# Optimization experiments

Hardware: AMD Instinct MI355X
Metric: run time of the kernel (lower is better)

The kernel has to match this reference:

```python
import jax, jax.numpy as jnp
import numpy as np

N_ENTITY = 64368
N_REL = 40
DIM = 128
NUM_BASES = 8
N_EDGES = 1_200_000
BATCH = 64
MAX_SEED = 32


def setup_inputs() -> dict:
    key = jax.random.key(0)
    ks = jax.random.split(key, 12)
    basis = jax.random.normal(ks[0], (NUM_BASES, N_ENTITY, DIM), jnp.float32) * 0.02
    att = jax.random.normal(ks[1], (N_REL, NUM_BASES), jnp.float32) * 0.1
    root = jax.random.normal(ks[2], (N_ENTITY, DIM), jnp.float32) * 0.02
    rgcn_bias = jnp.zeros((DIM,), jnp.float32)
    xav = 1.414 / np.sqrt(DIM)  # xavier_uniform gain=1.414 scale
    attn_a = jax.random.uniform(ks[3], (DIM, DIM), jnp.float32, -xav, xav)
    attn_b = jax.random.uniform(ks[4], (DIM, 1), jnp.float32, -xav, xav)
    output_bias = jnp.zeros((N_ENTITY,), jnp.float32)
    edge_index = jax.random.randint(ks[5], (2, N_EDGES), 0, N_ENTITY, jnp.int32)
    edge_type = jax.random.randint(ks[6], (N_EDGES,), 0, N_REL, jnp.int32)
    lengths = jax.random.randint(ks[7], (BATCH,), 1, MAX_SEED + 1, jnp.int32)
    seed_mask = jnp.arange(MAX_SEED)[None, :] < lengths[:, None]  # ragged seed sets
    seed_idx = jax.random.randint(ks[8], (BATCH, MAX_SEED), 0, N_ENTITY, jnp.int32)
    labels = jax.random.randint(ks[9], (BATCH,), 0, N_ENTITY, jnp.int32)
    return dict(basis=basis, att=att, root=root, rgcn_bias=rgcn_bias,
                attn_a=attn_a, attn_b=attn_b, output_bias=output_bias,
                edge_index=edge_index, edge_type=edge_type,
                seed_idx=seed_idx, seed_mask=seed_mask, labels=labels)


def reference(basis, att, root, rgcn_bias, attn_a, attn_b, output_bias,
              edge_index, edge_type, seed_idx, seed_mask, labels):
    # ---- RGCNConv with x=None (old PyG): msg_e = (att[rel_e] @ basis)[src_e] ----
    src, dst = edge_index[0], edge_index[1]
    coeff = att[edge_type]                      # [E, B]
    # loop over small fixed num_bases to avoid materializing [B, E, D]
    msg = coeff[:, 0:1] * basis[0][src]         # [E, D]
    for b in range(1, basis.shape[0]):
        msg = msg + coeff[:, b:b + 1] * basis[b][src]
    agg = jax.ops.segment_sum(msg, dst, num_segments=root.shape[0])  # scatter-add
    nodes = agg + root + rgcn_bias              # [N, D] node features

    # ---- per-seed-set gather + self-attention pooling ----
    h = nodes[seed_idx]                         # [Bt, L, D]
    e = jnp.squeeze(jnp.tanh(h @ attn_a) @ attn_b, -1)  # [Bt, L]
    e = jnp.where(seed_mask, e, -jnp.inf)
    attn = jax.nn.softmax(e, axis=-1)
    u = jnp.einsum('bl,bld->bd', attn, h)       # [Bt, D] user reps

    # ---- scores = F.linear(u, nodes, output.bias); CE loss ----
    scores = u @ nodes.T + output_bias          # [Bt, N]
    logp = jax.nn.log_softmax(scores, axis=-1)
    loss = -jnp.mean(jnp.take_along_axis(logp, labels[:, None].astype(jnp.int32), axis=1))
    return scores, loss
```

## Files before the change

kernel.cpp:

```cpp
#include <hip/hip_runtime.h>
#include <hip/hip_bf16.h>

#define N_ENT 64368
#define DIM 128
#define NB 8
#define NREL 40
#define BATCH 64
#define MAXSEED 32

__device__ __forceinline__ unsigned pack_bf2(float x, float y) {
    union { float f; unsigned u; } a, b;
    a.f = x; b.f = y;
    unsigned ra = a.u + 0x7FFFu + ((a.u >> 16) & 1u);
    unsigned rb = b.u + 0x7FFFu + ((b.u >> 16) & 1u);
    return (ra >> 16) | (rb & 0xFFFF0000u);
}

__global__ void mask_norm_kernel(const unsigned char* __restrict__ raw,
                                 int* __restrict__ outMask) {
    __shared__ int s_ni, s_nf;
    int t = threadIdx.x;
    if (t == 0) { s_ni = 0; s_nf = 0; }
    __syncthreads();
    const unsigned int* u32 = (const unsigned int*)raw;
    int not_int = 0, not_flt = 0;
    for (int i = t; i < 512; i += blockDim.x) {
        unsigned int g = u32[i];
        if (g != 0u && g != 1u) not_int = 1;
        if (g != 0u && g != 0x3F800000u) not_flt = 1;
    }
    if (not_int) atomicOr(&s_ni, 1);
    if (not_flt) atomicOr(&s_nf, 1);
    __syncthreads();
    int mode = (!s_ni) ? 0 : ((!s_nf) ? 1 : 2);
    for (int i = t; i < BATCH * MAXSEED; i += blockDim.x) {
        int v;
        if (mode == 0)      v = ((const int*)raw)[i] != 0;
        else if (mode == 1) v = (((const float*)raw)[i] != 0.0f);
        else                v = raw[i] != 0;
        outMask[i] = v;
    }
}

__global__ __launch_bounds__(256) void hist_kernel(
    const int* __restrict__ eidx, int E,
    int* __restrict__ cntS, int* __restrict__ cntD)
{
    int i = blockIdx.x * blockDim.x + threadIdx.x;
    int n = gridDim.x * blockDim.x;
    for (int e = i; e < E; e += n) {
        atomicAdd(&cntS[eidx[e]], 1);
        atomicAdd(&cntD[eidx[e + E]], 1);
    }
}

__global__ __launch_bounds__(1024) void scan2_kernel(
    const int* __restrict__ cntS, int* __restrict__ rpS, int* __restrict__ ofS,
    const int* __restrict__ cntD, int* __restrict__ rpD, int* __restrict__ ofD)
{
    const int* cnt = blockIdx.x ? cntD : cntS;
    int* row_ptr   = blockIdx.x ? rpD : rpS;
    int* ofs       = blockIdx.x ? ofD : ofS;
    __shared__ int s[1024];
    const int t = threadIdx.x;
    const int CH = 63;
    const int base = t * CH;
    int sum = 0;
    for (int j = 0; j < CH; ++j) { int p = base + j; if (p < N_ENT) sum += cnt[p]; }
    s[t] = sum;
    for (int off = 1; off < 1024; off <<= 1) {
        __syncthreads();
        int x = (t >= off) ? s[t - off] : 0;
        __syncthreads();
        s[t] += x;
    }
    __syncthreads();
    int run = s[t] - sum;
    for (int j = 0; j < CH; ++j) {
        int p = base + j;
        if (p < N_ENT) { row_ptr[p] = run; ofs[p] = run; run += cnt[p]; }
    }
    if (t == 1023) row_ptr[N_ENT] = s[1023];
}

__global__ __launch_bounds__(256) void scat2_kernel(
    const int* __restrict__ eidx, const int* __restrict__ etype, int E,
    int* __restrict__ ofsS, int* __restrict__ ofsD, int useDstRank,
    unsigned* __restrict__ srcSorted)
{
    int i = blockIdx.x * blockDim.x + threadIdx.x;
    int n = gridDim.x * blockDim.x;
    for (int e = i; e < E; e += n) {
        int s = eidx[e];
        int d = eidx[e + E];
        int p = atomicAdd(&ofsS[s], 1);
        unsigned hi = useDstRank ? (unsigned)atomicAdd(&ofsD[d], 1) : (unsigned)d;
        srcSorted[p] = (hi << 6) | (unsigned)etype[e];
    }
}

__global__ __launch_bounds__(256) void msg_kernel(
    const float* __restrict__ basis, const float* __restrict__ att,
    const int* __restrict__ row_ptrS, const unsigned* __restrict__ srcSorted,
    unsigned* __restrict__ msg)
{
    __shared__ float att_s[NREL * NB];
    const int t = threadIdx.x;
    for (int i = t; i < NREL * NB; i += 256) att_s[i] = att[i];
    __syncthreads();
    const int lane = t & 63;
    const int s = blockIdx.x * 4 + (t >> 6);
    const int r0 = row_ptrS[s], r1 = row_ptrS[s + 1];
    if (r0 == r1) return;
    float2 B[NB];
#pragma unroll
    for (int b = 0; b < NB; ++b)
        B[b] = ((const float2*)(basis + ((size_t)b * N_ENT + s) * DIM))[lane];
    for (int i = r0; i < r1; ++i) {
        unsigned pk = srcSorted[i];
        const float* __restrict__ c = att_s + (pk & 63u) * NB;
        size_t dp = (size_t)(pk >> 6);
        float mx = 0.f, my = 0.f;
#pragma unroll
        for (int b = 0; b < NB; ++b) { mx += c[b] * B[b].x; my += c[b] * B[b].y; }
        __builtin_nontemporal_store(pack_bf2(mx, my), msg + dp * 64 + lane);
    }
}

__global__ __launch_bounds__(256) void reduce_kernel(
    const unsigned* __restrict__ msg, const int* __restrict__ row_ptrD,
    const float* __restrict__ root, const float* __restrict__ rbias,
    float* __restrict__ nodes)
{
    const int t = threadIdx.x;
    const int lane = t & 63;
    const int d = blockIdx.x * 4 + (t >> 6);
    const int r0 = row_ptrD[d], r1 = row_ptrD[d + 1];
    float2 acc = ((const float2*)(root + (size_t)d * DIM))[lane];
    acc.x += rbias[lane * 2];
    acc.y += rbias[lane * 2 + 1];
    for (int i = r0; i < r1; ++i) {
        unsigned u = __builtin_nontemporal_load(msg + (size_t)i * 64 + lane);
        acc.x += __uint_as_float(u << 16);
        acc.y += __uint_as_float(u & 0xFFFF0000u);
    }
    ((float2*)(nodes + (size_t)d * DIM))[lane] = acc;
}

__global__ __launch_bounds__(256) void edge_atomic_kernel(
    const float* __restrict__ basis, const float* __restrict__ att,
    const int* __restrict__ row_ptrS, const unsigned* __restrict__ srcSorted,
    float* __restrict__ nodes)
{
    __shared__ float att_s[NREL * NB];
    const int t = threadIdx.x;
    for (int i = t; i < NREL * NB; i += 256) att_s[i] = att[i];
    __syncthreads();
    const int lane = t & 63;
    const int s = blockIdx.x * 4 + (t >> 6);
    const int r0 = row_ptrS[s], r1 = row_ptrS[s + 1];
    if (r0 == r1) return;
    float2 B[NB];
#pragma unroll
    for (int b = 0; b < NB; ++b)
        B[b] = ((const float2*)(basis + ((size_t)b * N_ENT + s) * DIM))[lane];
    for (int i = r0; i < r1; ++i) {
        unsigned pk = srcSorted[i];
        const float* __restrict__ c = att_s + (pk & 63u) * NB;
        int d = (int)(pk >> 6);
        float mx = 0.f, my = 0.f;
#pragma unroll
        for (int b = 0; b < NB; ++b) { mx += c[b] * B[b].x; my += c[b] * B[b].y; }
        float* dp = nodes + (size_t)d * DIM + lane * 2;
        unsafeAtomicAdd(dp, mx);
        unsafeAtomicAdd(dp + 1, my);
    }
}

__global__ __launch_bounds__(256) void finalize_nodes(
    float* __restrict__ nodes, const float* __restrict__ root,
    const float* __restrict__ bias, int total)
{
    int i = blockIdx.x * blockDim.x + threadIdx.x;
    if (i < total) nodes[i] = nodes[i] + root[i] + bias[i & (DIM - 1)];
}

__global__ __launch_bounds__(128) void attn_kernel(
    const float* __restrict__ nodes, const float* __restrict__ A,
    const float* __restrict__ bvec, const int* __restrict__ seed_idx,
    const int* __restrict__ maskN, float* __restrict__ u)
{
    __shared__ float A_s[DIM * DIM];
    __shared__ float h_s[MAXSEED * DIM];
    __shared__ float ev[MAXSEED];
    __shared__ float aw[MAXSEED];
    __shared__ float red[2];
    const int b = blockIdx.x;
    const int t = threadIdx.x;

    for (int i = t; i < DIM * DIM; i += 128) A_s[i] = A[i];
    for (int l = 0; l < MAXSEED; ++l) {
        int idx = seed_idx[b * MAXSEED + l];
        h_s[l * DIM + t] = nodes[(size_t)idx * DIM + t];
    }
    __syncthreads();

    const float bv = bvec[t];
    for (int l = 0; l < MAXSEED; ++l) {
        float s = 0.f;
#pragma unroll 8
        for (int d1 = 0; d1 < DIM; ++d1) s += h_s[l * DIM + d1] * A_s[d1 * DIM + t];
        float val = tanhf(s) * bv;
#pragma unroll
        for (int off = 32; off > 0; off >>= 1) val += __shfl_down(val, off, 64);
        if ((t & 63) == 0) red[t >> 6] = val;
        __syncthreads();
        if (t == 0) ev[l] = red[0] + red[1];
        __syncthreads();
    }

    if (t == 0) {
        float mx = -1e30f;
        for (int l = 0; l < MAXSEED; ++l)
            if (maskN[b * MAXSEED + l]) mx = fmaxf(mx, ev[l]);
        float den = 0.f;
        for (int l = 0; l < MAXSEED; ++l) {
            float w = maskN[b * MAXSEED + l] ? expf(ev[l] - mx) : 0.f;
            aw[l] = w;
            den += w;
        }
        float inv = 1.f / den;
        for (int l = 0; l < MAXSEED; ++l) aw[l] *= inv;
    }
    __syncthreads();

    float s = 0.f;
    for (int l = 0; l < MAXSEED; ++l) s += aw[l] * h_s[l * DIM + t];
    u[b * DIM + t] = s;
}

__global__ __launch_bounds__(256) void scores_kernel(
    const float* __restrict__ nodes, const float* __restrict__ u,
    const float* __restrict__ obias, float* __restrict__ out)
{
    __shared__ float u_s[BATCH * DIM];
    const int t = threadIdx.x;
    const int n0 = blockIdx.x * 64;
    for (int i = t; i < BATCH * DIM; i += 256) u_s[i] = u[i];
    __syncthreads();
    const int nl = t & 63, bg = t >> 6;
    const int n = n0 + nl;
    const int nc = n < N_ENT ? n : N_ENT - 1;
    const float4* __restrict__ nrow = (const float4*)(nodes + (size_t)nc * DIM);
    float acc[16];
#pragma unroll
    for (int bi = 0; bi < 16; ++bi) acc[bi] = 0.f;
    for (int dc = 0; dc < DIM / 4; ++dc) {
        const float4 nr = nrow[dc];
#pragma unroll
        for (int bi = 0; bi < 16; ++bi) {
            const float4 uu = *(const float4*)(u_s + (bg * 16 + bi) * DIM + dc * 4);
            acc[bi] += nr.x * uu.x + nr.y * uu.y + nr.z * uu.z + nr.w * uu.w;
        }
    }
    if (n < N_ENT) {
        const float ob = obias[n];
#pragma unroll
        for (int bi = 0; bi < 16; ++bi)
            out[(size_t)(bg * 16 + bi) * N_ENT + n] = acc[bi] + ob;
    }
}

#define LSE_CH 8
__global__ __launch_bounds__(256) void lse1_kernel(
    const float* __restrict__ scores, float2* __restrict__ pls)
{
    const int b = blockIdx.x >> 3, c = blockIdx.x & 7;
    const int t = threadIdx.x;
    const int CH = (N_ENT + LSE_CH - 1) / LSE_CH;
    const int i0 = c * CH, i1 = min(N_ENT, i0 + CH);
    const float* __restrict__ row = scores + (size_t)b * N_ENT;
    __shared__ float red[4], red2[4];
    float mx = -1e30f;
    for (int i = i0 + t; i < i1; i += 256) mx = fmaxf(mx, row[i]);
#pragma unroll
    for (int off = 32; off > 0; off >>= 1) mx = fmaxf(mx, __shfl_down(mx, off, 64));
    if ((t & 63) == 0) red[t >> 6] = mx;
    __syncthreads();
    const float m4 = fmaxf(fmaxf(red[0], red[1]), fmaxf(red[2], red[3]));
    float ss = 0.f;
    for (int i = i0 + t; i < i1; i += 256) ss += expf(row[i] - m4);
#pragma unroll
    for (int off = 32; off > 0; off >>= 1) ss += __shfl_down(ss, off, 64);
    if ((t & 63) == 0) red2[t >> 6] = ss;
    __syncthreads();
    if (t == 0) pls[blockIdx.x] = make_float2(m4, red2[0] + red2[1] + red2[2] + red2[3]);
}

__global__ void lse2_kernel(const float2* __restrict__ pls, float* __restrict__ lse)
{
    const int b = threadIdx.x;
    if (b < BATCH) {
        float M = -1e30f;
        for (int c = 0; c < LSE_CH; ++c) M = fmaxf(M, pls[b * LSE_CH + c].x);
        float S = 0.f;
        for (int c = 0; c < LSE_CH; ++c) {
            float2 p = pls[b * LSE_CH + c];
            S += p.y * expf(p.x - M);
        }
        lse[b] = M + logf(S);
    }
}

__global__ void loss_kernel(const float* __restrict__ scores,
                            const float* __restrict__ lse,
                            const int* __restrict__ labels,
                            float* __restrict__ out_loss)
{
    const int t = threadIdx.x;
    float v = 0.f;
    if (t < BATCH) {
        int lab = labels[t];
        v = lse[t] - scores[(size_t)t * N_ENT + lab];
    }
#pragma unroll
    for (int off = 32; off > 0; off >>= 1) v += __shfl_down(v, off, 64);
    if (t == 0) out_loss[0] = v * (1.0f / BATCH);
}

extern "C" void kernel_launch(void* const* d_in, const int* in_sizes, int n_in,
                              void* d_out, int out_size, void* d_ws, size_t ws_size,
                              hipStream_t stream) {
    const float* basis = (const float*)d_in[0];
    const float* att   = (const float*)d_in[1];
    const float* root  = (const float*)d_in[2];
    const float* rbias = (const float*)d_in[3];
    const float* attnA = (const float*)d_in[4];
    const float* attnB = (const float*)d_in[5];
    const float* obias = (const float*)d_in[6];
    const int* eindex  = (const int*)d_in[7];
    const int* etype   = (const int*)d_in[8];
    const int* sidx    = (const int*)d_in[9];
    const unsigned char* smask = (const unsigned char*)d_in[10];
    const int* labels  = (const int*)d_in[11];
    const int E = in_sizes[8];
    float* out = (float*)d_out;

    auto alignup = [](size_t x) { return (x + 511) & ~(size_t)511; };
    char* p = (char*)d_ws;
    float* nodes = (float*)p;      p += alignup((size_t)N_ENT * DIM * 4);
    float* u     = (float*)p;      p += alignup((size_t)BATCH * DIM * 4);
    float* lse   = (float*)p;      p += alignup(BATCH * 4);
    float2* pls  = (float2*)p;     p += alignup(BATCH * LSE_CH * 8);
    int* maskN   = (int*)p;        p += alignup(BATCH * MAXSEED * 4);
    int* cntS    = (int*)p;
    int* cntD    = cntS + N_ENT;   p += alignup((size_t)2 * N_ENT * 4);
    int* row_ptrS= (int*)p;        p += alignup((size_t)(N_ENT + 1) * 4);
    int* ofsS    = (int*)p;        p += alignup((size_t)N_ENT * 4);
    int* row_ptrD= (int*)p;        p += alignup((size_t)(N_ENT + 1) * 4);
    int* ofsD    = (int*)p;        p += alignup((size_t)N_ENT * 4);
    unsigned* srcSorted = (unsigned*)p; p += alignup((size_t)E * 4);
    unsigned* msg = (unsigned*)p;  p += alignup((size_t)E * 64 * 4);
    const bool planA = ((size_t)(p - (char*)d_ws) <= ws_size);

    const int eb = (E + 255) / 256;
    const int egrid = eb > 2048 ? 2048 : eb;

    mask_norm_kernel<<<1, 256, 0, stream>>>(smask, maskN);
    hipMemsetAsync(cntS, 0, (size_t)2 * N_ENT * 4, stream);
    hist_kernel<<<egrid, 256, 0, stream>>>(eindex, E, cntS, cntD);
    scan2_kernel<<<2, 1024, 0, stream>>>(cntS, row_ptrS, ofsS, cntD, row_ptrD, ofsD);

    if (planA) {
        scat2_kernel<<<egrid, 256, 0, stream>>>(eindex, etype, E, ofsS, ofsD, 1, srcSorted);
        msg_kernel<<<N_ENT / 4, 256, 0, stream>>>(basis, att, row_ptrS, srcSorted, msg);
        reduce_kernel<<<N_ENT / 4, 256, 0, stream>>>(msg, row_ptrD, root, rbias, nodes);
    } else {
        hipMemsetAsync(nodes, 0, (size_t)N_ENT * DIM * 4, stream);
        scat2_kernel<<<egrid, 256, 0, stream>>>(eindex, etype, E, ofsS, ofsD, 0, srcSorted);
        edge_atomic_kernel<<<N_ENT / 4, 256, 0, stream>>>(basis, att, row_ptrS, srcSorted, nodes);
        finalize_nodes<<<((N_ENT * DIM) + 255) / 256, 256, 0, stream>>>(nodes, root, rbias, N_ENT * DIM);
    }

    attn_kernel<<<BATCH, 128, 0, stream>>>(nodes, attnA, attnB, sidx, maskN, u);
    scores_kernel<<<(N_ENT + 63) / 64, 256, 0, stream>>>(nodes, u, obias, out);
    lse1_kernel<<<BATCH * LSE_CH, 256, 0, stream>>>(out, pls);
    lse2_kernel<<<1, 64, 0, stream>>>(pls, lse);
    loss_kernel<<<1, 64, 0, stream>>>(out, lse, labels, out + (size_t)BATCH * N_ENT);
}
```

Baseline: 1.114 ms.

## Pad offset counters, vectorize edge loads, move dst-rank atomics into msg kernel

Offset counters are padded to 64 bytes apart so that atomics on different nodes no longer contend on the same cache line. The histogram and scatter kernels now handle four edges per thread with int4 loads. The destination-rank atomic moves out of the scatter pass into the message kernel, where one lane per edge claims the slot and the result is shuffled to the wavefront. This removes one atomic per edge from scatter, but puts atomic latency on the msg kernel's critical path, and the padded counters take 16x more memory.

```diff
diff --git a/kernel.cpp b/kernel.cpp
--- a/kernel.cpp
+++ b/kernel.cpp
@@ -7,6 +7,7 @@
 #define NREL 40
 #define BATCH 64
 #define MAXSEED 32
+#define OPAD 16
 
 __device__ __forceinline__ unsigned pack_bf2(float x, float y) {
     union { float f; unsigned u; } a, b;
@@ -46,11 +47,20 @@
     const int* __restrict__ eidx, int E,
     int* __restrict__ cntS, int* __restrict__ cntD)
 {
-    int i = blockIdx.x * blockDim.x + threadIdx.x;
-    int n = gridDim.x * blockDim.x;
-    for (int e = i; e < E; e += n) {
-        atomicAdd(&cntS[eidx[e]], 1);
-        atomicAdd(&cntD[eidx[e + E]], 1);
+    const int t = blockIdx.x * blockDim.x + threadIdx.x;
+    const int e0 = t * 4;
+    if (((E & 3) == 0) && e0 + 3 < E) {
+        int4 s4 = *(const int4*)(eidx + e0);
+        int4 d4 = *(const int4*)(eidx + E + e0);
+        atomicAdd(&cntS[s4.x], 1); atomicAdd(&cntS[s4.y], 1);
+        atomicAdd(&cntS[s4.z], 1); atomicAdd(&cntS[s4.w], 1);
+        atomicAdd(&cntD[d4.x], 1); atomicAdd(&cntD[d4.y], 1);
+        atomicAdd(&cntD[d4.z], 1); atomicAdd(&cntD[d4.w], 1);
+    } else {
+        for (int e = e0; e < E && e < e0 + 4; ++e) {
+            atomicAdd(&cntS[eidx[e]], 1);
+            atomicAdd(&cntD[eidx[e + E]], 1);
+        }
     }
 }
 
@@ -78,31 +88,41 @@
     int run = s[t] - sum;
     for (int j = 0; j < CH; ++j) {
         int p = base + j;
-        if (p < N_ENT) { row_ptr[p] = run; ofs[p] = run; run += cnt[p]; }
+        if (p < N_ENT) { row_ptr[p] = run; ofs[(size_t)p * OPAD] = run; run += cnt[p]; }
     }
     if (t == 1023) row_ptr[N_ENT] = s[1023];
 }
 
-__global__ __launch_bounds__(256) void scat2_kernel(
+__global__ __launch_bounds__(256) void scatS_kernel(
     const int* __restrict__ eidx, const int* __restrict__ etype, int E,
-    int* __restrict__ ofsS, int* __restrict__ ofsD, int useDstRank,
-    unsigned* __restrict__ srcSorted)
-{
-    int i = blockIdx.x * blockDim.x + threadIdx.x;
-    int n = gridDim.x * blockDim.x;
-    for (int e = i; e < E; e += n) {
-        int s = eidx[e];
-        int d = eidx[e + E];
-        int p = atomicAdd(&ofsS[s], 1);
-        unsigned hi = useDstRank ? (unsigned)atomicAdd(&ofsD[d], 1) : (unsigned)d;
-        srcSorted[p] = (hi << 6) | (unsigned)etype[e];
+    int* __restrict__ ofsS, unsigned* __restrict__ srcSorted)
+{
+    const int t = blockIdx.x * blockDim.x + threadIdx.x;
+    const int e0 = t * 4;
+    if (((E & 3) == 0) && e0 + 3 < E) {
+        int4 s4 = *(const int4*)(eidx + e0);
+        int4 d4 = *(const int4*)(eidx + E + e0);
+        int4 r4 = *(const int4*)(etype + e0);
+        int p0 = atomicAdd(&ofsS[(size_t)s4.x * OPAD], 1);
+        int p1 = atomicAdd(&ofsS[(size_t)s4.y * OPAD], 1);
+        int p2 = atomicAdd(&ofsS[(size_t)s4.z * OPAD], 1);
+        int p3 = atomicAdd(&ofsS[(size_t)s4.w * OPAD], 1);
+        srcSorted[p0] = ((unsigned)d4.x << 6) | (unsigned)r4.x;
+        srcSorted[p1] = ((unsigned)d4.y << 6) | (unsigned)r4.y;
+        srcSorted[p2] = ((unsigned)d4.z << 6) | (unsigned)r4.z;
+        srcSorted[p3] = ((unsigned)d4.w << 6) | (unsigned)r4.w;
+    } else {
+        for (int e = e0; e < E && e < e0 + 4; ++e) {
+            int p = atomicAdd(&ofsS[(size_t)eidx[e] * OPAD], 1);
+            srcSorted[p] = ((unsigned)eidx[e + E] << 6) | (unsigned)etype[e];
+        }
     }
 }
 
 __global__ __launch_bounds__(256) void msg_kernel(
     const float* __restrict__ basis, const float* __restrict__ att,
     const int* __restrict__ row_ptrS, const unsigned* __restrict__ srcSorted,
-    unsigned* __restrict__ msg)
+    int* __restrict__ ofsD, unsigned* __restrict__ msg)
 {
     __shared__ float att_s[NREL * NB];
     const int t = threadIdx.x;
@@ -116,14 +136,20 @@
 #pragma unroll
     for (int b = 0; b < NB; ++b)
         B[b] = ((const float2*)(basis + ((size_t)b * N_ENT + s) * DIM))[lane];
-    for (int i = r0; i < r1; ++i) {
-        unsigned pk = srcSorted[i];
-        const float* __restrict__ c = att_s + (pk & 63u) * NB;
-        size_t dp = (size_t)(pk >> 6);
-        float mx = 0.f, my = 0.f;
-#pragma unroll
-        for (int b = 0; b < NB; ++b) { mx += c[b] * B[b].x; my += c[b] * B[b].y; }
-        __builtin_nontemporal_store(pack_bf2(mx, my), msg + dp * 64 + lane);
+    for (int i = r0; i < r1; i += 4) {
+        const int m = min(4, r1 - i);
+        unsigned pk_l = (lane < m) ? srcSorted[i + lane] : 0u;
+        int q_l = 0;
+        if (lane < m) q_l = atomicAdd(&ofsD[(size_t)(pk_l >> 6) * OPAD], 1);
+        for (int j = 0; j < m; ++j) {
+            unsigned pk = (unsigned)__shfl((int)pk_l, j, 64);
+            int q = __shfl(q_l, j, 64);
+            const float* __restrict__ c = att_s + (pk & 63u) * NB;
+            float mx = 0.f, my = 0.f;
+#pragma unroll
+            for (int b = 0; b < NB; ++b) { mx += c[b] * B[b].x; my += c[b] * B[b].y; }
+            __builtin_nontemporal_store(pack_bf2(mx, my), msg + (size_t)q * 64 + lane);
+        }
     }
 }
 
@@ -356,28 +382,26 @@
     int* cntS    = (int*)p;
     int* cntD    = cntS + N_ENT;   p += alignup((size_t)2 * N_ENT * 4);
     int* row_ptrS= (int*)p;        p += alignup((size_t)(N_ENT + 1) * 4);
-    int* ofsS    = (int*)p;        p += alignup((size_t)N_ENT * 4);
     int* row_ptrD= (int*)p;        p += alignup((size_t)(N_ENT + 1) * 4);
-    int* ofsD    = (int*)p;        p += alignup((size_t)N_ENT * 4);
+    int* ofsS    = (int*)p;        p += alignup((size_t)N_ENT * OPAD * 4);
+    int* ofsD    = (int*)p;        p += alignup((size_t)N_ENT * OPAD * 4);
     unsigned* srcSorted = (unsigned*)p; p += alignup((size_t)E * 4);
     unsigned* msg = (unsigned*)p;  p += alignup((size_t)E * 64 * 4);
     const bool planA = ((size_t)(p - (char*)d_ws) <= ws_size);
 
-    const int eb = (E + 255) / 256;
-    const int egrid = eb > 2048 ? 2048 : eb;
+    const int gridE4 = ((E + 3) / 4 + 255) / 256;
 
     mask_norm_kernel<<<1, 256, 0, stream>>>(smask, maskN);
     hipMemsetAsync(cntS, 0, (size_t)2 * N_ENT * 4, stream);
-    hist_kernel<<<egrid, 256, 0, stream>>>(eindex, E, cntS, cntD);
+    hist_kernel<<<gridE4, 256, 0, stream>>>(eindex, E, cntS, cntD);
     scan2_kernel<<<2, 1024, 0, stream>>>(cntS, row_ptrS, ofsS, cntD, row_ptrD, ofsD);
+    scatS_kernel<<<gridE4, 256, 0, stream>>>(eindex, etype, E, ofsS, srcSorted);
 
     if (planA) {
-        scat2_kernel<<<egrid, 256, 0, stream>>>(eindex, etype, E, ofsS, ofsD, 1, srcSorted);
-        msg_kernel<<<N_ENT / 4, 256, 0, stream>>>(basis, att, row_ptrS, srcSorted, msg);
+        msg_kernel<<<N_ENT / 4, 256, 0, stream>>>(basis, att, row_ptrS, srcSorted, ofsD, msg);
         reduce_kernel<<<N_ENT / 4, 256, 0, stream>>>(msg, row_ptrD, root, rbias, nodes);
     } else {
         hipMemsetAsync(nodes, 0, (size_t)N_ENT * DIM * 4, stream);
-        scat2_kernel<<<egrid, 256, 0, stream>>>(eindex, etype, E, ofsS, ofsD, 0, srcSorted);
         edge_atomic_kernel<<<N_ENT / 4, 256, 0, stream>>>(basis, att, row_ptrS, srcSorted, nodes);
         finalize_nodes<<<((N_ENT * DIM) + 255) / 256, 256, 0, stream>>>(nodes, root, rbias, N_ENT * DIM);
     }
```

After: 1.041 ms. 6.6% less time.
